# Performance work log

Measured on AMD Instinct MI355X. Metric: run time of the kernel, lower is better.

Reference implementation:

```python
import jax, jax.numpy as jnp
import numpy as np

N, L, S, E, A, D = 16, 256, 128, 128, 9, 768
ARG_ROLES = 23      # score width = ARG_ROLES + 1
MAX_ARG = 9         # hard-coded max_len_arg in the torch module
N_HID = 768


def setup_inputs() -> dict:
    key = jax.random.key(0)
    ks = jax.random.split(key, 10)
    all_embeddings = jax.random.normal(ks[0], (N, L, D), jnp.float32)
    # last-3-layer BERT attention maps, 12 heads, positive entries
    attn_last3 = jax.random.uniform(ks[1], (3, N, 12, L, L), jnp.float32)
    # per-sample sorted distinct first-subword indices (all positive, full length:
    # the ragged filter idxs>0 then keeps everything -> fixed-shape gather)
    idx_keys = jax.random.split(ks[2], N)
    cand = jnp.arange(1, L - MAX_ARG - 1)
    idxs_to_collect = jax.vmap(
        lambda k: jnp.sort(jax.random.choice(k, cand, (S + 2,), replace=False))
    )(idx_keys).astype(jnp.int32)
    is_triggers = (jax.random.uniform(ks[3], (N, S)) < 0.05).astype(jnp.float32)
    is_triggers = is_triggers.at[:, 0].set(1.0)  # >=1 trigger per sample
    entity_mapping = jax.random.normal(ks[4], (N, S, E), jnp.float32) * 0.05
    arg_weight_matrices = jax.random.normal(ks[5], (N, MAX_ARG, A), jnp.float32) * 0.3
    map_keys = jax.random.split(ks[6], N)
    arg_mapping = jax.vmap(
        lambda k: jax.random.permutation(k, ARG_ROLES + 1)[:A]
    )(map_keys).astype(jnp.int32)
    W1 = jax.random.normal(ks[7], (6 * D, N_HID), jnp.float32) * 0.02
    b1 = jnp.zeros((N_HID,), jnp.float32)
    W2 = jax.random.normal(ks[8], (N_HID, 1), jnp.float32) * 0.02
    b2 = jnp.zeros((1,), jnp.float32)
    return {
        "all_embeddings": all_embeddings,
        "attn_last3": attn_last3,
        "entity_mapping": entity_mapping,
        "arg_weight_matrices": arg_weight_matrices,
        "is_triggers": is_triggers,
        "W1": W1, "b1": b1, "W2": W2, "b2": b2,
        "idxs_to_collect": idxs_to_collect,
        "arg_mapping": arg_mapping,
    }


def reference(all_embeddings, attn_last3, entity_mapping, arg_weight_matrices,
              is_triggers, W1, b1, W2, b2, idxs_to_collect, arg_mapping):
    sqrt_d = jnp.sqrt(jnp.asarray(D, jnp.float32))
    sent_idx = idxs_to_collect[:, :S]                      # [N,S] first-subword ids
    # get_fist_subword_embeddings: ragged gather (full-length here)
    sent_emb = jnp.take_along_axis(all_embeddings, sent_idx[:, :, None], axis=1)  # [N,S,D]
    # arg-type tokens sit right after the second-to-last [SEP]
    arg_pos = idxs_to_collect[:, -2:-1] + 1 + jnp.arange(MAX_ARG)[None, :]        # [N,9]
    arg_raw = jnp.take_along_axis(all_embeddings, arg_pos[:, :, None], axis=1)    # [N,9,D]

    entity_emb = jnp.einsum('nsd,nse->ned', sent_emb, entity_mapping)             # [N,E,D]
    trig = jnp.sum(sent_emb * is_triggers[..., None], axis=1) \
           / jnp.sum(is_triggers, axis=1, keepdims=True)                          # [N,D]
    del trig  # _trigger is computed but unused downstream in the torch forward
    arg_emb = jnp.einsum('nkd,nka->nad', arg_raw, arg_weight_matrices)            # [N,A,D]

    # bi-attention scores (broadcast-mul-sum == contraction over D)
    t2a = jnp.einsum('ned,nad->nea', entity_emb, arg_emb) / sqrt_d
    w = (t2a - 5.0) / 2.0                                                         # [N,E,A]
    token_argAwared = jnp.einsum('nea,nad->ned', w, arg_emb)                      # [N,E,D]
    arg_tokenAwared = jnp.einsum('nea,ned->nad', w, entity_emb)                   # [N,A,D]

    # select_hidden_att for each of the last 3 layers
    att_mean = jnp.mean(attn_last3, axis=2)                                       # [3,N,L,L]
    def sel_layer(a):  # a: [N,L,L] -> row/col gather + row renorm
        s = jax.vmap(lambda m, i: m[i][:, i])(a, sent_idx)                        # [N,S,S]
        return s / (jnp.sum(s, axis=-1, keepdims=True) + 1e-9)
    t2t = (sel_layer(att_mean[0]) + sel_layer(att_mean[1]) + sel_layer(att_mean[2])) / 3.0

    h2h_sent = jnp.einsum('nst,ntd->nsd', t2t, sent_emb)                          # [N,S,D]
    # A_h2h and H_ are projected from sent space (S) to entity space (E)
    A_h2h_e = jnp.einsum('nsd,nse->ned', h2h_sent, entity_mapping)                # [N,E,D]
    H_e = entity_emb                                                              # sent_emb projected == entity_emb

    a2a = jax.nn.softmax(jnp.einsum('nad,nbd->nab', arg_emb, arg_emb), axis=-1)   # [N,A,A]
    u2u = jnp.einsum('nab,nbd->nad', a2a, arg_emb)                                # [N,A,D]

    shp = (N, E, A, D)
    H_    = jnp.broadcast_to(H_e[:, :, None, :], shp)
    U_    = jnp.broadcast_to(arg_emb[:, None, :, :], shp)
    A_h2u = jnp.broadcast_to(token_argAwared[:, :, None, :], shp)
    A_h2h = jnp.broadcast_to(A_h2h_e[:, :, None, :], shp)
    A_u2h = jnp.broadcast_to(arg_tokenAwared[:, None, :, :], shp)
    A_u2u = jnp.broadcast_to(u2u[:, None, :, :], shp)
    latent = jnp.concatenate([H_, U_, A_h2u, A_h2h, A_u2h, A_u2u], axis=-1)       # [N,E,A,6D]

    hid = jax.nn.gelu(latent @ W1 + b1, approximate=False)                        # [N,E,A,768]
    score = (hid @ W2 + b2)[..., 0]                                               # [N,E,A]

    # map_arg_to_ids: scatter each arg slot back to its global role id
    def scatter_one(s, ids):  # s [E,A], ids [A]
        return jnp.full((E, ARG_ROLES + 1), -1e6, jnp.float32).at[:, ids].set(s)
    new_score = jax.vmap(scatter_one)(score, arg_mapping)                         # [N,E,24]
    return new_score
```

## Files before the change

### kernel.cpp

```cpp
#include <hip/hip_runtime.h>
#include <math.h>

namespace {
constexpr int N_ = 16, L_ = 256, S_ = 128, E_ = 128, A_ = 9, D_ = 768, H_ = 768, RO_ = 24;
constexpr int IDXW = 130;
constexpr int W1R = 6 * D_;
constexpr float INV_SQRT_D = 0.03608439182435161f;
constexpr int PESZ = 2048 * 768;
constexpr int PASZ = 144 * 768;
constexpr int GB_T2T    = 0;
constexpr int GB_W1T    = 1024;
constexpr int GB_GATHER = 1888;
constexpr int GB_ENTMAP = 2080;
constexpr int GB_ARGU   = 2096;
constexpr int GB_TOTAL  = 2112;
}

using bshort8 = __attribute__((ext_vector_type(8))) short;
using f32x4v = __attribute__((ext_vector_type(4))) float;

__device__ __forceinline__ unsigned short f2bf(float f) {
    unsigned u = __builtin_bit_cast(unsigned, f);
    return (unsigned short)((u + 0x7fffu + ((u >> 16) & 1u)) >> 16);
}

__device__ __forceinline__ void gemm_body128(const unsigned short* __restrict__ A,
                                             const unsigned short* __restrict__ BT,
                                             int lda, int ldb, int c0, int tid,
                                             short (*As)[40], short (*Bs)[40],
                                             f32x4v acc[2][4]) {
    const int wave = tid >> 6, lane = tid & 63;
    const int row16 = lane & 15, quad = lane >> 4;
    for (int k0 = 0; k0 < S_; k0 += 32) {
#pragma unroll
        for (int i = 0; i < 2; ++i) {
            const int idx = tid + 256 * i;
            const int r = idx >> 2, q = idx & 3;
            *reinterpret_cast<bshort8*>(&As[r][q * 8]) =
                *reinterpret_cast<const bshort8*>(A + (size_t)r * lda + k0 + q * 8);
        }
        {
            const int col = tid >> 2, q = tid & 3;
            *reinterpret_cast<bshort8*>(&Bs[col][q * 8]) =
                *reinterpret_cast<const bshort8*>(BT + (size_t)(c0 + col) * ldb + k0 + q * 8);
        }
        __syncthreads();
        bshort8 a[2], b[4];
#pragma unroll
        for (int mi = 0; mi < 2; ++mi)
            a[mi] = *reinterpret_cast<const bshort8*>(&As[wave * 32 + mi * 16 + row16][quad * 8]);
#pragma unroll
        for (int ni = 0; ni < 4; ++ni)
            b[ni] = *reinterpret_cast<const bshort8*>(&Bs[ni * 16 + row16][quad * 8]);
#pragma unroll
        for (int mi = 0; mi < 2; ++mi)
#pragma unroll
            for (int ni = 0; ni < 4; ++ni)
                acc[mi][ni] = __builtin_amdgcn_mfma_f32_16x16x32_bf16(a[mi], b[ni], acc[mi][ni], 0, 0, 0);
        __syncthreads();
    }
}

__global__ __launch_bounds__(256) void stage1_k(const float* __restrict__ all_emb,
                                                const int* __restrict__ idxs,
                                                const float* __restrict__ ent_map,
                                                const float* __restrict__ W1,
                                                const float* __restrict__ argw,
                                                const float* __restrict__ attn,
                                                unsigned short* __restrict__ sentT,
                                                unsigned short* __restrict__ entmapT,
                                                short* __restrict__ W1t,
                                                unsigned short* __restrict__ t2tT,
                                                float* __restrict__ argE,
                                                unsigned short* __restrict__ argEbf,
                                                unsigned short* __restrict__ u2ubf) {
    __shared__ __align__(16) unsigned char smem[33792];
    const int b = blockIdx.x, tid = threadIdx.x;

    if (b < GB_W1T) {
        const int idx = b - GB_T2T;
        const int n = idx >> 6;
        const int half = tid >> 7, t128 = tid & 127;
        const int s0 = (idx & 63) << 1;
        const int s = s0 | half;
        const int w = t128 >> 6, lane = tid & 63;
        float* sum2 = (float*)smem;
        float* part = (float*)(smem + 12288);
        unsigned short* tileT = (unsigned short*)(smem + 12544);
        const int is = idxs[n * IDXW + s], it = idxs[n * IDXW + t128];
#pragma unroll
        for (int l = 0; l < 3; ++l) {
            const float* base = attn + ((size_t)((l * N_ + n) * 12 + w * 6)) * (L_ * L_)
                              + (size_t)is * L_ + lane * 4;
            float4 acc = {0.f, 0.f, 0.f, 0.f};
#pragma unroll
            for (int h = 0; h < 6; ++h) {
                const float4 v = *reinterpret_cast<const float4*>(base + (size_t)h * (L_ * L_));
                acc.x += v.x; acc.y += v.y; acc.z += v.z; acc.w += v.w;
            }
            *reinterpret_cast<float4*>(&sum2[(((half * 3 + l) * 2 + w) << 8) + lane * 4]) = acc;
        }
        __syncthreads();
        float m[3];
#pragma unroll
        for (int l = 0; l < 3; ++l) {
            m[l] = (sum2[(((half * 3 + l) * 2 + 0) << 8) + it] +
                    sum2[(((half * 3 + l) * 2 + 1) << 8) + it]) * (1.0f / 12.0f);
            float r = m[l];
#pragma unroll
            for (int off = 32; off; off >>= 1) r += __shfl_xor(r, off, 64);
            if (lane == 0) part[(half * 3 + l) * 2 + w] = r;
        }
        __syncthreads();
        float out = 0.f;
#pragma unroll
        for (int l = 0; l < 3; ++l)
            out += m[l] / (part[(half * 3 + l) * 2 + 0] + part[(half * 3 + l) * 2 + 1] + 1e-9f);
        tileT[t128 * 2 + half] = f2bf(out * (1.0f / 3.0f));
        __syncthreads();
        if (tid < 128) {
            const unsigned int v = ((const unsigned int*)tileT)[tid];
            *reinterpret_cast<unsigned int*>(t2tT + ((size_t)(n * S_) + tid) * S_ + s0) = v;
        }
    } else if (b < GB_GATHER) {
        const int b2 = b - GB_W1T;
        const int k0 = (b2 % 72) * 64, h0 = (b2 / 72) * 64;
        auto tile = (float (*)[65])smem;
        const int tx = tid & 63, ty = tid >> 6;
#pragma unroll
        for (int i = 0; i < 16; ++i) {
            const int r = ty + i * 4;
            tile[r][tx] = W1[(size_t)(k0 + r) * H_ + h0 + tx];
        }
        __syncthreads();
#pragma unroll
        for (int i = 0; i < 16; ++i) {
            const int r = ty + i * 4;
            W1t[(size_t)(h0 + r) * W1R + k0 + tx] = (short)f2bf(tile[tx][r]);
        }
    } else if (b < GB_ENTMAP) {
        const int b2 = b - GB_GATHER;
        const int n = b2 / 12, d0 = (b2 % 12) * 64;
        auto tile = (unsigned short (*)[132])smem;
#pragma unroll
        for (int it = 0; it < 8; ++it) {
            const int lin = tid + 256 * it;
            const int s = lin >> 4, dq = (lin & 15) * 4;
            const int row = idxs[n * IDXW + s];
            const float4 v = *reinterpret_cast<const float4*>(all_emb + ((size_t)(n * L_ + row)) * D_ + d0 + dq);
            tile[dq + 0][s] = f2bf(v.x); tile[dq + 1][s] = f2bf(v.y);
            tile[dq + 2][s] = f2bf(v.z); tile[dq + 3][s] = f2bf(v.w);
        }
        __syncthreads();
#pragma unroll
        for (int it = 0; it < 8; ++it) {
            const int lin = tid + 256 * it;
            const int d = lin >> 5, s4 = (lin & 31) * 4;
            ushort4 v = {tile[d][s4], tile[d][s4 + 1], tile[d][s4 + 2], tile[d][s4 + 3]};
            *reinterpret_cast<ushort4*>(sentT + ((size_t)(n * D_) + d0 + d) * S_ + s4) = v;
        }
    } else if (b < GB_ARGU) {
        const int n = b - GB_ENTMAP;
        auto tile = (unsigned short (*)[132])smem;
#pragma unroll
        for (int it = 0; it < 16; ++it) {
            const int lin = tid + 256 * it;
            const int s = lin >> 5, eq = (lin & 31) * 4;
            const float4 v = *reinterpret_cast<const float4*>(ent_map + ((size_t)(n * S_ + s)) * E_ + eq);
            tile[eq + 0][s] = f2bf(v.x); tile[eq + 1][s] = f2bf(v.y);
            tile[eq + 2][s] = f2bf(v.z); tile[eq + 3][s] = f2bf(v.w);
        }
        __syncthreads();
#pragma unroll
        for (int it = 0; it < 16; ++it) {
            const int lin = tid + 256 * it;
            const int e = lin >> 5, s4 = (lin & 31) * 4;
            ushort4 v = {tile[e][s4], tile[e][s4 + 1], tile[e][s4 + 2], tile[e][s4 + 3]};
            *reinterpret_cast<ushort4*>(entmapT + ((size_t)(n * E_) + e) * S_ + s4) = v;
        }
    } else {
        const int n = b - GB_ARGU;
        auto wsm = (float (*)[A_])smem;
        auto part45 = (float (*)[4])(smem + 512);
        auto Psm = (float (*)[A_])(smem + 1536);
        if (tid < A_ * A_) wsm[tid / A_][tid % A_] = argw[n * A_ * A_ + tid];
        __syncthreads();
        const int p0 = idxs[n * IDXW + S_] + 1;
        float pp[45] = {};
        float vals[3][A_];
#pragma unroll
        for (int c = 0; c < 3; ++c) {
            const int d = tid + 256 * c;
            float raw[A_];
#pragma unroll
            for (int k = 0; k < A_; ++k) raw[k] = all_emb[((size_t)(n * L_ + p0 + k)) * D_ + d];
#pragma unroll
            for (int a = 0; a < A_; ++a) {
                float acc = 0.f;
#pragma unroll
                for (int k = 0; k < A_; ++k) acc = fmaf(raw[k], wsm[k][a], acc);
                vals[c][a] = acc;
                argE[((size_t)(n * A_ + a)) * D_ + d] = acc;
                argEbf[((size_t)(n * A_ + a)) * D_ + d] = f2bf(acc);
            }
            int p = 0;
#pragma unroll
            for (int a = 0; a < A_; ++a)
#pragma unroll
                for (int bb = a; bb < A_; ++bb) pp[p++] += vals[c][a] * vals[c][bb];
        }
        const int lane = tid & 63, wv = tid >> 6;
#pragma unroll
        for (int p = 0; p < 45; ++p) {
            float v = pp[p];
            for (int off = 32; off; off >>= 1) v += __shfl_down(v, off, 64);
            if (lane == 0) part45[p][wv] = v;
        }
        __syncthreads();
        if (tid < 45) part45[tid][0] = part45[tid][0] + part45[tid][1] + part45[tid][2] + part45[tid][3];
        __syncthreads();
        if (tid < A_) {
            const int a = tid;
            float v[A_], mx = -1e30f;
#pragma unroll
            for (int bb = 0; bb < A_; ++bb) {
                const int lo = a < bb ? a : bb, hi = a < bb ? bb : a;
                v[bb] = part45[lo * (19 - lo) / 2 + hi - lo][0];
                mx = fmaxf(mx, v[bb]);
            }
            float sm = 0.f;
#pragma unroll
            for (int bb = 0; bb < A_; ++bb) { v[bb] = expf(v[bb] - mx); sm += v[bb]; }
            const float inv = 1.0f / sm;
#pragma unroll
            for (int bb = 0; bb < A_; ++bb) Psm[a][bb] = v[bb] * inv;
        }
        __syncthreads();
#pragma unroll
        for (int c = 0; c < 3; ++c) {
            const int d = tid + 256 * c;
#pragma unroll
            for (int a = 0; a < A_; ++a) {
                float acc = 0.f;
#pragma unroll
                for (int bb = 0; bb < A_; ++bb) acc = fmaf(Psm[a][bb], vals[c][bb], acc);
                u2ubf[((size_t)(n * A_ + a)) * D_ + d] = f2bf(acc);
            }
        }
    }
}

__global__ __launch_bounds__(256) void gemm_entM1_k(const unsigned short* __restrict__ entmapT,
                                                    const unsigned short* __restrict__ sentT,
                                                    const unsigned short* __restrict__ t2tT,
                                                    float* __restrict__ entf,
                                                    unsigned short* __restrict__ entbf,
                                                    unsigned short* __restrict__ M1bf) {
    __shared__ __align__(16) short As[128][40];
    __shared__ __align__(16) short Bs[64][40];
    const int bx = blockIdx.x, tid = threadIdx.x;
    const int wave = tid >> 6, lane = tid & 63;
    const int row16 = lane & 15, quad = lane >> 4;
    f32x4v acc[2][4] = {};
    if (bx < 192) {
        const int n = bx / 12, c0 = (bx % 12) * 64;
        gemm_body128(entmapT + (size_t)n * S_ * S_, sentT + (size_t)n * D_ * S_,
                     S_, S_, c0, tid, As, Bs, acc);
#pragma unroll
        for (int mi = 0; mi < 2; ++mi)
#pragma unroll
            for (int ni = 0; ni < 4; ++ni) {
                const int rbase = wave * 32 + mi * 16 + quad * 4;
                const int col = c0 + ni * 16 + row16;
#pragma unroll
                for (int t = 0; t < 4; ++t) {
                    const size_t o = ((size_t)(n * S_) + rbase + t) * D_ + col;
                    entf[o] = acc[mi][ni][t];
                    entbf[o] = f2bf(acc[mi][ni][t]);
                }
            }
    } else {
        const int idx = bx - 192;
        const int n = idx >> 1, c0 = (idx & 1) * 64;
        gemm_body128(entmapT + (size_t)n * S_ * S_, t2tT + (size_t)n * S_ * S_,
                     S_, S_, c0, tid, As, Bs, acc);
#pragma unroll
        for (int mi = 0; mi < 2; ++mi)
#pragma unroll
            for (int ni = 0; ni < 4; ++ni) {
                const int rbase = wave * 32 + mi * 16 + quad * 4;
                const int col = c0 + ni * 16 + row16;
#pragma unroll
                for (int t = 0; t < 4; ++t)
                    M1bf[((size_t)(n * S_) + rbase + t) * S_ + col] = f2bf(acc[mi][ni][t]);
            }
    }
}

__global__ __launch_bounds__(256) void fused3_k(const unsigned short* __restrict__ M1bf,
                                                const unsigned short* __restrict__ sentT,
                                                const float* __restrict__ entf,
                                                const float* __restrict__ argE,
                                                unsigned short* __restrict__ Ah2hbf,
                                                unsigned short* __restrict__ tokAbf,
                                                unsigned short* __restrict__ argTbf) {
    __shared__ __align__(16) unsigned char smem[15872];
    const int bx = blockIdx.x, tid = threadIdx.x;
    if (bx < N_ * A_) {
        const int n = bx / A_, a = bx % A_;
        float* argS = (float*)smem;
        float* wl = (float*)(smem + 3072);
        for (int i = tid; i < D_; i += 256) argS[i] = argE[((size_t)(n * A_ + a)) * D_ + i];
        __syncthreads();
        {
            const int e = tid >> 1, h = tid & 1;
            const float* er = entf + ((size_t)(n * E_ + e)) * D_ + h * 384;
            float p = 0.f;
            for (int d = 0; d < 384; ++d) p = fmaf(er[d], argS[h * 384 + d], p);
            p += __shfl_down(p, 1, 64);
            if (h == 0) wl[e] = (p * INV_SQRT_D - 5.0f) * 0.5f;
        }
        __syncthreads();
        const float* eb = entf + (size_t)n * E_ * D_;
#pragma unroll
        for (int c = 0; c < 3; ++c) {
            const int d = tid + 256 * c;
            float acc = 0.f;
            for (int e = 0; e < E_; ++e) acc = fmaf(wl[e], eb[(size_t)e * D_ + d], acc);
            argTbf[((size_t)(n * A_ + a)) * D_ + d] = f2bf(acc);
        }
    } else if (bx < N_ * A_ + 192) {
        const int idx = bx - N_ * A_;
        const int n = idx / 12, c0 = (idx % 12) * 64;
        short (*As)[40] = (short (*)[40])smem;
        short (*Bs)[40] = (short (*)[40])(smem + 10240);
        const int wave = tid >> 6, lane = tid & 63;
        const int row16 = lane & 15, quad = lane >> 4;
        f32x4v acc[2][4] = {};
        gemm_body128(M1bf + (size_t)n * S_ * S_, sentT + (size_t)n * D_ * S_,
                     S_, S_, c0, tid, As, Bs, acc);
#pragma unroll
        for (int mi = 0; mi < 2; ++mi)
#pragma unroll
            for (int ni = 0; ni < 4; ++ni) {
                const int rbase = wave * 32 + mi * 16 + quad * 4;
                const int col = c0 + ni * 16 + row16;
#pragma unroll
                for (int t = 0; t < 4; ++t)
                    Ah2hbf[((size_t)(n * S_) + rbase + t) * D_ + col] = f2bf(acc[mi][ni][t]);
            }
    } else {
        const int idx = bx - (N_ * A_ + 192);
        const int n = idx >> 7, e = idx & 127;
        float* wl = (float*)smem;
        float* part = (float*)(smem + 64);
        const float* er = entf + ((size_t)(n * E_ + e)) * D_;
        const float* ar = argE + (size_t)n * A_ * D_;
        float acc[A_] = {};
        for (int d = tid; d < D_; d += 256) {
            const float ev = er[d];
#pragma unroll
            for (int a = 0; a < A_; ++a) acc[a] = fmaf(ev, ar[(size_t)a * D_ + d], acc[a]);
        }
        const int lane = tid & 63, wv = tid >> 6;
#pragma unroll
        for (int a = 0; a < A_; ++a)
            for (int off = 32; off; off >>= 1) acc[a] += __shfl_down(acc[a], off, 64);
        if (lane == 0)
            for (int a = 0; a < A_; ++a) part[a * 4 + wv] = acc[a];
        __syncthreads();
        if (tid < A_)
            wl[tid] = ((part[tid * 4] + part[tid * 4 + 1] + part[tid * 4 + 2] + part[tid * 4 + 3])
                       * INV_SQRT_D - 5.0f) * 0.5f;
        __syncthreads();
#pragma unroll
        for (int c = 0; c < 3; ++c) {
            const int d = tid + 256 * c;
            float s = 0.f;
#pragma unroll
            for (int a = 0; a < A_; ++a) s = fmaf(wl[a], ar[(size_t)a * D_ + d], s);
            tokAbf[((size_t)(n * E_ + e)) * D_ + d] = f2bf(s);
        }
    }
}

__global__ __launch_bounds__(256) void mfma_mlp_k(const unsigned short* __restrict__ e0,
                                                  const unsigned short* __restrict__ e1,
                                                  const unsigned short* __restrict__ e2,
                                                  const unsigned short* __restrict__ a0,
                                                  const unsigned short* __restrict__ a1,
                                                  const unsigned short* __restrict__ a2,
                                                  const short* __restrict__ W1t,
                                                  float* __restrict__ Pe3, float* __restrict__ Pa3) {
    __shared__ __align__(16) short As[128][40];
    __shared__ __align__(16) short Bs[64][40];
    const int c0 = blockIdx.x * 64;
    const int by = blockIdx.y;
    const int seg = by / 18;
    const int blk = by % 18;
    const bool isPa = blk >= 16;
    const unsigned short* Aseg;
    int woff;
    if (isPa) {
        Aseg = seg == 0 ? a0 : (seg == 1 ? a1 : a2);
        woff = seg == 0 ? 1 * D_ : (seg == 1 ? 4 * D_ : 5 * D_);
    } else {
        Aseg = seg == 0 ? e0 : (seg == 1 ? e1 : e2);
        woff = seg == 0 ? 0 : (seg == 1 ? 2 * D_ : 3 * D_);
    }
    const int M = isPa ? N_ * A_ : N_ * E_;
    const int r0 = (isPa ? blk - 16 : blk) * 128;
    float* C = isPa ? (Pa3 + (size_t)seg * PASZ) : (Pe3 + (size_t)seg * PESZ);
    const int tid = threadIdx.x;
    const int wave = tid >> 6, lane = tid & 63;
    const int row16 = lane & 15, quad = lane >> 4;
    f32x4v acc[2][4] = {};
    for (int kk = 0; kk < D_; kk += 32) {
#pragma unroll
        for (int i = 0; i < 2; ++i) {
            const int idx = tid + 256 * i;
            const int r = idx >> 2, q = idx & 3;
            bshort8 av = {};
            if (r0 + r < M) av = *reinterpret_cast<const bshort8*>(Aseg + (size_t)(r0 + r) * D_ + kk + q * 8);
            *reinterpret_cast<bshort8*>(&As[r][q * 8]) = av;
        }
        {
            const int col = tid >> 2, q = tid & 3;
            *reinterpret_cast<bshort8*>(&Bs[col][q * 8]) =
                *reinterpret_cast<const bshort8*>(W1t + (size_t)(c0 + col) * W1R + woff + kk + q * 8);
        }
        __syncthreads();
        bshort8 a[2], b[4];
#pragma unroll
        for (int mi = 0; mi < 2; ++mi)
            a[mi] = *reinterpret_cast<const bshort8*>(&As[wave * 32 + mi * 16 + row16][quad * 8]);
#pragma unroll
        for (int ni = 0; ni < 4; ++ni)
            b[ni] = *reinterpret_cast<const bshort8*>(&Bs[ni * 16 + row16][quad * 8]);
#pragma unroll
        for (int mi = 0; mi < 2; ++mi)
#pragma unroll
            for (int ni = 0; ni < 4; ++ni)
                acc[mi][ni] = __builtin_amdgcn_mfma_f32_16x16x32_bf16(a[mi], b[ni], acc[mi][ni], 0, 0, 0);
        __syncthreads();
    }
#pragma unroll
    for (int mi = 0; mi < 2; ++mi) {
#pragma unroll
        for (int ni = 0; ni < 4; ++ni) {
            const int rbase = r0 + wave * 32 + mi * 16 + quad * 4;
            const int col = c0 + ni * 16 + row16;
#pragma unroll
            for (int t = 0; t < 4; ++t)
                if (rbase + t < M) C[(size_t)(rbase + t) * H_ + col] = acc[mi][ni][t];
        }
    }
}

__global__ __launch_bounds__(256) void score_k(const float* __restrict__ Pe3, const float* __restrict__ Pa3,
                                               const float* __restrict__ b1, const float* __restrict__ W2,
                                               const float* __restrict__ b2, const int* __restrict__ arg_map,
                                               float* __restrict__ out) {
    const int n = blockIdx.x >> 7, e = blockIdx.x & 127;
    const int tid = threadIdx.x;
    __shared__ float paS[A_ * H_];
    __shared__ float part[A_][4];
    float* orow = out + ((size_t)(n * E_ + e)) * RO_;
    if (tid < RO_) orow[tid] = -1000000.0f;
    for (int i = tid; i < A_ * H_; i += 256) {
        const size_t o = (size_t)n * A_ * H_ + i;
        paS[i] = Pa3[o] + Pa3[PASZ + o] + Pa3[2 * PASZ + o];
    }
    __syncthreads();
    const size_t ro = ((size_t)(n * E_ + e)) * H_;
    float acc[A_] = {};
    for (int h = tid; h < H_; h += 256) {
        const float pe = Pe3[ro + h] + Pe3[PESZ + ro + h] + Pe3[2 * PESZ + ro + h] + b1[h];
        const float w2 = W2[h];
#pragma unroll
        for (int a = 0; a < A_; ++a) {
            const float x = pe + paS[a * H_ + h];
            const float g = x * 0.5f * (1.0f + erff(x * 0.70710678118654752f));
            acc[a] = fmaf(g, w2, acc[a]);
        }
    }
    const int lane = tid & 63, wv = tid >> 6;
#pragma unroll
    for (int a = 0; a < A_; ++a)
        for (int off = 32; off; off >>= 1) acc[a] += __shfl_down(acc[a], off, 64);
    if (lane == 0)
        for (int a = 0; a < A_; ++a) part[a][wv] = acc[a];
    __syncthreads();
    if (tid < A_) {
        const float s = part[tid][0] + part[tid][1] + part[tid][2] + part[tid][3] + b2[0];
        orow[arg_map[n * A_ + tid]] = s;
    }
}

extern "C" void kernel_launch(void* const* d_in, const int* in_sizes, int n_in,
                              void* d_out, int out_size, void* d_ws, size_t ws_size,
                              hipStream_t stream) {
    const float* all_emb = (const float*)d_in[0];
    const float* attn    = (const float*)d_in[1];
    const float* ent_map = (const float*)d_in[2];
    const float* argw    = (const float*)d_in[3];
    const float* W1 = (const float*)d_in[5];
    const float* b1 = (const float*)d_in[6];
    const float* W2 = (const float*)d_in[7];
    const float* b2 = (const float*)d_in[8];
    const int* idxs    = (const int*)d_in[9];
    const int* arg_map = (const int*)d_in[10];
    float* out = (float*)d_out;

    float* ws = (float*)d_ws;
    float* entf = ws + 0;
    float* Pe3  = ws + 1572864;
    float* argE = ws + 6291456;
    float* Pa3  = ws + 6402048;
    short*          W1t     = (short*)(ws + 6733824);
    unsigned short* sentT   = (unsigned short*)(ws + 8503296);
    unsigned short* entmapT = (unsigned short*)(ws + 9289728);
    unsigned short* t2tT    = (unsigned short*)(ws + 9420800);
    unsigned short* M1bf    = (unsigned short*)(ws + 9551872);
    unsigned short* argEbf  = (unsigned short*)(ws + 9682944);
    unsigned short* u2ubf   = (unsigned short*)(ws + 9738240);
    unsigned short* entbf   = (unsigned short*)(ws + 9793536);
    unsigned short* Ah2hbf  = (unsigned short*)(ws + 10579968);
    unsigned short* tokAbf  = (unsigned short*)(ws + 11366400);
    unsigned short* argTbf  = (unsigned short*)(ws + 12152832);

    stage1_k<<<GB_TOTAL, 256, 0, stream>>>(all_emb, idxs, ent_map, W1, argw, attn,
                                           sentT, entmapT, W1t, t2tT, argE, argEbf, u2ubf);

    gemm_entM1_k<<<224, 256, 0, stream>>>(entmapT, sentT, t2tT, entf, entbf, M1bf);

    fused3_k<<<N_ * A_ + 192 + N_ * E_, 256, 0, stream>>>(M1bf, sentT, entf, argE,
                                                          Ah2hbf, tokAbf, argTbf);

    mfma_mlp_k<<<dim3(12, 54), 256, 0, stream>>>(entbf, tokAbf, Ah2hbf, argEbf, argTbf, u2ubf, W1t, Pe3, Pa3);

    score_k<<<N_ * E_, 256, 0, stream>>>(Pe3, Pa3, b1, W2, b2, arg_map, out);

    (void)in_sizes; (void)n_in; (void)out_size; (void)ws_size;
}
```

Before: 329.7 us.

## Split fused stage into MFMA attention-score GEMM and post kernel, fast erf

Replaces the old fused3 kernel with two kernels. The first computes the entity-argument similarity weights once with bf16 MFMA into a small buffer, alongside the Ah2h GEMM tiles. The second uses those weights for both token-aware and arg-aware products, so the redundant per-block fp32 dot products are gone. It also swaps erff in the GELU for an Abramowitz-Stegun polynomial, splits the entmap transpose into more blocks with smaller shared memory, and reorders the MLP grid so segments are interleaved. The risks are an extra launch, bf16 precision in the similarity scores, and about 1e-7 approximation error in erf.

```diff
diff --git a/kernel.cpp b/kernel.cpp
--- a/kernel.cpp
+++ b/kernel.cpp
@@ -12,8 +12,8 @@
 constexpr int GB_W1T    = 1024;
 constexpr int GB_GATHER = 1888;
 constexpr int GB_ENTMAP = 2080;
-constexpr int GB_ARGU   = 2096;
-constexpr int GB_TOTAL  = 2112;
+constexpr int GB_ARGU   = 2112;
+constexpr int GB_TOTAL  = 2128;
 }
 
 using bshort8 = __attribute__((ext_vector_type(8))) short;
@@ -22,6 +22,18 @@
 __device__ __forceinline__ unsigned short f2bf(float f) {
     unsigned u = __builtin_bit_cast(unsigned, f);
     return (unsigned short)((u + 0x7fffu + ((u >> 16) & 1u)) >> 16);
+}
+
+__device__ __forceinline__ float erf_fast(float x) {
+    const float ax = fabsf(x);
+    const float t = 1.0f / fmaf(0.3275911f, ax, 1.0f);
+    float p = fmaf(1.061405429f, t, -1.453152027f);
+    p = fmaf(p, t, 1.421413741f);
+    p = fmaf(p, t, -0.284496736f);
+    p = fmaf(p, t, 0.254829592f);
+    p = p * t;
+    const float r = 1.0f - p * __expf(-ax * ax);
+    return copysignf(r, x);
 }
 
 __device__ __forceinline__ void gemm_body128(const unsigned short* __restrict__ A,
@@ -74,7 +86,7 @@
                                                 float* __restrict__ argE,
                                                 unsigned short* __restrict__ argEbf,
                                                 unsigned short* __restrict__ u2ubf) {
-    __shared__ __align__(16) unsigned char smem[33792];
+    __shared__ __align__(16) unsigned char smem[16896];
     const int b = blockIdx.x, tid = threadIdx.x;
 
     if (b < GB_W1T) {
@@ -112,11 +124,11 @@
             if (lane == 0) part[(half * 3 + l) * 2 + w] = r;
         }
         __syncthreads();
-        float out = 0.f;
+        float o = 0.f;
 #pragma unroll
         for (int l = 0; l < 3; ++l)
-            out += m[l] / (part[(half * 3 + l) * 2 + 0] + part[(half * 3 + l) * 2 + 1] + 1e-9f);
-        tileT[t128 * 2 + half] = f2bf(out * (1.0f / 3.0f));
+            o += m[l] / (part[(half * 3 + l) * 2 + 0] + part[(half * 3 + l) * 2 + 1] + 1e-9f);
+        tileT[t128 * 2 + half] = f2bf(o * (1.0f / 3.0f));
         __syncthreads();
         if (tid < 128) {
             const unsigned int v = ((const unsigned int*)tileT)[tid];
@@ -160,23 +172,24 @@
             *reinterpret_cast<ushort4*>(sentT + ((size_t)(n * D_) + d0 + d) * S_ + s4) = v;
         }
     } else if (b < GB_ARGU) {
-        const int n = b - GB_ENTMAP;
+        const int idx = b - GB_ENTMAP;
+        const int n = idx >> 1, e0 = (idx & 1) * 64;
         auto tile = (unsigned short (*)[132])smem;
 #pragma unroll
-        for (int it = 0; it < 16; ++it) {
+        for (int it = 0; it < 8; ++it) {
             const int lin = tid + 256 * it;
-            const int s = lin >> 5, eq = (lin & 31) * 4;
-            const float4 v = *reinterpret_cast<const float4*>(ent_map + ((size_t)(n * S_ + s)) * E_ + eq);
+            const int s = lin >> 4, eq = (lin & 15) * 4;
+            const float4 v = *reinterpret_cast<const float4*>(ent_map + ((size_t)(n * S_ + s)) * E_ + e0 + eq);
             tile[eq + 0][s] = f2bf(v.x); tile[eq + 1][s] = f2bf(v.y);
             tile[eq + 2][s] = f2bf(v.z); tile[eq + 3][s] = f2bf(v.w);
         }
         __syncthreads();
 #pragma unroll
-        for (int it = 0; it < 16; ++it) {
+        for (int it = 0; it < 8; ++it) {
             const int lin = tid + 256 * it;
             const int e = lin >> 5, s4 = (lin & 31) * 4;
             ushort4 v = {tile[e][s4], tile[e][s4 + 1], tile[e][s4 + 2], tile[e][s4 + 3]};
-            *reinterpret_cast<ushort4*>(entmapT + ((size_t)(n * E_) + e) * S_ + s4) = v;
+            *reinterpret_cast<ushort4*>(entmapT + ((size_t)(n * E_) + e0 + e) * S_ + s4) = v;
         }
     } else {
         const int n = b - GB_ARGU;
@@ -250,12 +263,12 @@
     }
 }
 
-__global__ __launch_bounds__(256) void gemm_entM1_k(const unsigned short* __restrict__ entmapT,
-                                                    const unsigned short* __restrict__ sentT,
-                                                    const unsigned short* __restrict__ t2tT,
-                                                    float* __restrict__ entf,
-                                                    unsigned short* __restrict__ entbf,
-                                                    unsigned short* __restrict__ M1bf) {
+__global__ __launch_bounds__(256) void gemm_pair_k(const unsigned short* __restrict__ entmapT,
+                                                   const unsigned short* __restrict__ sentT,
+                                                   const unsigned short* __restrict__ t2tT,
+                                                   float* __restrict__ entf,
+                                                   unsigned short* __restrict__ entbf,
+                                                   unsigned short* __restrict__ M1bf) {
     __shared__ __align__(16) short As[128][40];
     __shared__ __align__(16) short Bs[64][40];
     const int bx = blockIdx.x, tid = threadIdx.x;
@@ -297,29 +310,85 @@
     }
 }
 
-__global__ __launch_bounds__(256) void fused3_k(const unsigned short* __restrict__ M1bf,
-                                                const unsigned short* __restrict__ sentT,
-                                                const float* __restrict__ entf,
-                                                const float* __restrict__ argE,
-                                                unsigned short* __restrict__ Ah2hbf,
-                                                unsigned short* __restrict__ tokAbf,
-                                                unsigned short* __restrict__ argTbf) {
-    __shared__ __align__(16) unsigned char smem[15872];
+__global__ __launch_bounds__(256) void gemm2_k(const unsigned short* __restrict__ M1bf,
+                                               const unsigned short* __restrict__ sentT,
+                                               const unsigned short* __restrict__ entbf,
+                                               const unsigned short* __restrict__ argEbf,
+                                               unsigned short* __restrict__ Ah2hbf,
+                                               float* __restrict__ wbuf) {
     const int bx = blockIdx.x, tid = threadIdx.x;
-    if (bx < N_ * A_) {
-        const int n = bx / A_, a = bx % A_;
-        float* argS = (float*)smem;
-        float* wl = (float*)(smem + 3072);
-        for (int i = tid; i < D_; i += 256) argS[i] = argE[((size_t)(n * A_ + a)) * D_ + i];
-        __syncthreads();
-        {
-            const int e = tid >> 1, h = tid & 1;
-            const float* er = entf + ((size_t)(n * E_ + e)) * D_ + h * 384;
-            float p = 0.f;
-            for (int d = 0; d < 384; ++d) p = fmaf(er[d], argS[h * 384 + d], p);
-            p += __shfl_down(p, 1, 64);
-            if (h == 0) wl[e] = (p * INV_SQRT_D - 5.0f) * 0.5f;
-        }
+    const int wave = tid >> 6, lane = tid & 63;
+    const int row16 = lane & 15, quad = lane >> 4;
+    if (bx < 192) {
+        __shared__ __align__(16) short As[128][40];
+        __shared__ __align__(16) short Bs[64][40];
+        const int n = bx / 12, c0 = (bx % 12) * 64;
+        f32x4v acc[2][4] = {};
+        gemm_body128(M1bf + (size_t)n * S_ * S_, sentT + (size_t)n * D_ * S_,
+                     S_, S_, c0, tid, As, Bs, acc);
+#pragma unroll
+        for (int mi = 0; mi < 2; ++mi)
+#pragma unroll
+            for (int ni = 0; ni < 4; ++ni) {
+                const int rbase = wave * 32 + mi * 16 + quad * 4;
+                const int col = c0 + ni * 16 + row16;
+#pragma unroll
+                for (int t = 0; t < 4; ++t)
+                    Ah2hbf[((size_t)(n * S_) + rbase + t) * D_ + col] = f2bf(acc[mi][ni][t]);
+            }
+    } else {
+        const int n = bx - 192;
+        const unsigned short* Aent = entbf + (size_t)n * E_ * D_;
+        const unsigned short* Barg = argEbf + (size_t)n * A_ * D_;
+        f32x4v acc[2] = {};
+        for (int k0 = 0; k0 < D_; k0 += 32) {
+            bshort8 a[2], bb;
+#pragma unroll
+            for (int mi = 0; mi < 2; ++mi)
+                a[mi] = *reinterpret_cast<const bshort8*>(Aent + (size_t)(wave * 32 + mi * 16 + row16) * D_ + k0 + quad * 8);
+            bb = *reinterpret_cast<const bshort8*>(Barg + (size_t)row16 * D_ + k0 + quad * 8);
+#pragma unroll
+            for (int mi = 0; mi < 2; ++mi)
+                acc[mi] = __builtin_amdgcn_mfma_f32_16x16x32_bf16(a[mi], bb, acc[mi], 0, 0, 0);
+        }
+        if (row16 < A_) {
+#pragma unroll
+            for (int mi = 0; mi < 2; ++mi)
+#pragma unroll
+                for (int t = 0; t < 4; ++t) {
+                    const int e = wave * 32 + mi * 16 + quad * 4 + t;
+                    const float w = (acc[mi][t] * INV_SQRT_D - 5.0f) * 0.5f;
+                    wbuf[((size_t)(n * E_ + e)) * A_ + row16] = w;
+                }
+        }
+    }
+}
+
+__global__ __launch_bounds__(256) void post_k(const float* __restrict__ wbuf,
+                                              const float* __restrict__ argE,
+                                              const float* __restrict__ entf,
+                                              unsigned short* __restrict__ tokAbf,
+                                              unsigned short* __restrict__ argTbf) {
+    const int b = blockIdx.x, tid = threadIdx.x;
+    if (b < N_ * E_) {
+        const int n = b >> 7, e = b & 127;
+        __shared__ float wl[A_];
+        if (tid < A_) wl[tid] = wbuf[(size_t)(n * E_ + e) * A_ + tid];
+        __syncthreads();
+        const float* ar = argE + (size_t)n * A_ * D_;
+#pragma unroll
+        for (int c = 0; c < 3; ++c) {
+            const int d = tid + 256 * c;
+            float s = 0.f;
+#pragma unroll
+            for (int a = 0; a < A_; ++a) s = fmaf(wl[a], ar[(size_t)a * D_ + d], s);
+            tokAbf[((size_t)(n * E_ + e)) * D_ + d] = f2bf(s);
+        }
+    } else {
+        const int idx = b - N_ * E_;
+        const int n = idx / A_, a = idx % A_;
+        __shared__ float wl[E_];
+        if (tid < E_) wl[tid] = wbuf[(size_t)(n * E_ + tid) * A_ + a];
         __syncthreads();
         const float* eb = entf + (size_t)n * E_ * D_;
 #pragma unroll
@@ -328,58 +397,6 @@
             float acc = 0.f;
             for (int e = 0; e < E_; ++e) acc = fmaf(wl[e], eb[(size_t)e * D_ + d], acc);
             argTbf[((size_t)(n * A_ + a)) * D_ + d] = f2bf(acc);
-        }
-    } else if (bx < N_ * A_ + 192) {
-        const int idx = bx - N_ * A_;
-        const int n = idx / 12, c0 = (idx % 12) * 64;
-        short (*As)[40] = (short (*)[40])smem;
-        short (*Bs)[40] = (short (*)[40])(smem + 10240);
-        const int wave = tid >> 6, lane = tid & 63;
-        const int row16 = lane & 15, quad = lane >> 4;
-        f32x4v acc[2][4] = {};
-        gemm_body128(M1bf + (size_t)n * S_ * S_, sentT + (size_t)n * D_ * S_,
-                     S_, S_, c0, tid, As, Bs, acc);
-#pragma unroll
-        for (int mi = 0; mi < 2; ++mi)
-#pragma unroll
-            for (int ni = 0; ni < 4; ++ni) {
-                const int rbase = wave * 32 + mi * 16 + quad * 4;
-                const int col = c0 + ni * 16 + row16;
-#pragma unroll
-                for (int t = 0; t < 4; ++t)
-                    Ah2hbf[((size_t)(n * S_) + rbase + t) * D_ + col] = f2bf(acc[mi][ni][t]);
-            }
-    } else {
-        const int idx = bx - (N_ * A_ + 192);
-        const int n = idx >> 7, e = idx & 127;
-        float* wl = (float*)smem;
-        float* part = (float*)(smem + 64);
-        const float* er = entf + ((size_t)(n * E_ + e)) * D_;
-        const float* ar = argE + (size_t)n * A_ * D_;
-        float acc[A_] = {};
-        for (int d = tid; d < D_; d += 256) {
-            const float ev = er[d];
-#pragma unroll
-            for (int a = 0; a < A_; ++a) acc[a] = fmaf(ev, ar[(size_t)a * D_ + d], acc[a]);
-        }
-        const int lane = tid & 63, wv = tid >> 6;
-#pragma unroll
-        for (int a = 0; a < A_; ++a)
-            for (int off = 32; off; off >>= 1) acc[a] += __shfl_down(acc[a], off, 64);
-        if (lane == 0)
-            for (int a = 0; a < A_; ++a) part[a * 4 + wv] = acc[a];
-        __syncthreads();
-        if (tid < A_)
-            wl[tid] = ((part[tid * 4] + part[tid * 4 + 1] + part[tid * 4 + 2] + part[tid * 4 + 3])
-                       * INV_SQRT_D - 5.0f) * 0.5f;
-        __syncthreads();
-#pragma unroll
-        for (int c = 0; c < 3; ++c) {
-            const int d = tid + 256 * c;
-            float s = 0.f;
-#pragma unroll
-            for (int a = 0; a < A_; ++a) s = fmaf(wl[a], ar[(size_t)a * D_ + d], s);
-            tokAbf[((size_t)(n * E_ + e)) * D_ + d] = f2bf(s);
         }
     }
 }
@@ -394,10 +411,9 @@
                                                   float* __restrict__ Pe3, float* __restrict__ Pa3) {
     __shared__ __align__(16) short As[128][40];
     __shared__ __align__(16) short Bs[64][40];
-    const int c0 = blockIdx.x * 64;
-    const int by = blockIdx.y;
-    const int seg = by / 18;
-    const int blk = by % 18;
+    const int bx = blockIdx.x;
+    const int seg = bx % 3;
+    const int blk = bx / 3;
     const bool isPa = blk >= 16;
     const unsigned short* Aseg;
     int woff;
@@ -411,6 +427,7 @@
     const int M = isPa ? N_ * A_ : N_ * E_;
     const int r0 = (isPa ? blk - 16 : blk) * 128;
     float* C = isPa ? (Pa3 + (size_t)seg * PASZ) : (Pe3 + (size_t)seg * PESZ);
+    const int c0 = blockIdx.y * 64;
     const int tid = threadIdx.x;
     const int wave = tid >> 6, lane = tid & 63;
     const int row16 = lane & 15, quad = lane >> 4;
@@ -480,7 +497,7 @@
 #pragma unroll
         for (int a = 0; a < A_; ++a) {
             const float x = pe + paS[a * H_ + h];
-            const float g = x * 0.5f * (1.0f + erff(x * 0.70710678118654752f));
+            const float g = x * 0.5f * (1.0f + erf_fast(x * 0.70710678118654752f));
             acc[a] = fmaf(g, w2, acc[a]);
         }
     }
@@ -516,28 +533,30 @@
     float* entf = ws + 0;
     float* Pe3  = ws + 1572864;
     float* argE = ws + 6291456;
-    float* Pa3  = ws + 6402048;
-    short*          W1t     = (short*)(ws + 6733824);
-    unsigned short* sentT   = (unsigned short*)(ws + 8503296);
-    unsigned short* entmapT = (unsigned short*)(ws + 9289728);
-    unsigned short* t2tT    = (unsigned short*)(ws + 9420800);
-    unsigned short* M1bf    = (unsigned short*)(ws + 9551872);
-    unsigned short* argEbf  = (unsigned short*)(ws + 9682944);
-    unsigned short* u2ubf   = (unsigned short*)(ws + 9738240);
-    unsigned short* entbf   = (unsigned short*)(ws + 9793536);
-    unsigned short* Ah2hbf  = (unsigned short*)(ws + 10579968);
-    unsigned short* tokAbf  = (unsigned short*)(ws + 11366400);
-    unsigned short* argTbf  = (unsigned short*)(ws + 12152832);
+    float* wbuf = ws + 6402048;
+    float* Pa3  = ws + 6420480;
+    short*          W1t     = (short*)(ws + 6752256);
+    unsigned short* sentT   = (unsigned short*)(ws + 8521728);
+    unsigned short* entmapT = (unsigned short*)(ws + 9308160);
+    unsigned short* t2tT    = (unsigned short*)(ws + 9439232);
+    unsigned short* M1bf    = (unsigned short*)(ws + 9570304);
+    unsigned short* argEbf  = (unsigned short*)(ws + 9701376);
+    unsigned short* u2ubf   = (unsigned short*)(ws + 9756672);
+    unsigned short* entbf   = (unsigned short*)(ws + 9811968);
+    unsigned short* Ah2hbf  = (unsigned short*)(ws + 10598400);
+    unsigned short* tokAbf  = (unsigned short*)(ws + 11384832);
+    unsigned short* argTbf  = (unsigned short*)(ws + 12171264);
 
     stage1_k<<<GB_TOTAL, 256, 0, stream>>>(all_emb, idxs, ent_map, W1, argw, attn,
                                            sentT, entmapT, W1t, t2tT, argE, argEbf, u2ubf);
 
-    gemm_entM1_k<<<224, 256, 0, stream>>>(entmapT, sentT, t2tT, entf, entbf, M1bf);
-
-    fused3_k<<<N_ * A_ + 192 + N_ * E_, 256, 0, stream>>>(M1bf, sentT, entf, argE,
-                                                          Ah2hbf, tokAbf, argTbf);
-
-    mfma_mlp_k<<<dim3(12, 54), 256, 0, stream>>>(entbf, tokAbf, Ah2hbf, argEbf, argTbf, u2ubf, W1t, Pe3, Pa3);
+    gemm_pair_k<<<224, 256, 0, stream>>>(entmapT, sentT, t2tT, entf, entbf, M1bf);
+
+    gemm2_k<<<208, 256, 0, stream>>>(M1bf, sentT, entbf, argEbf, Ah2hbf, wbuf);
+
+    post_k<<<N_ * E_ + N_ * A_, 256, 0, stream>>>(wbuf, argE, entf, tokAbf, argTbf);
+
+    mfma_mlp_k<<<dim3(54, H_ / 64), 256, 0, stream>>>(entbf, tokAbf, Ah2hbf, argEbf, argTbf, u2ubf, W1t, Pe3, Pa3);
 
     score_k<<<N_ * E_, 256, 0, stream>>>(Pe3, Pa3, b1, W2, b2, arg_map, out);
 
```

New measurement: 319.8 us. -3.0%, faster.
